# Performance work log

Measured on AMD Instinct MI355X. Metric: run time of the kernel, lower is better.

The kernel has to match this reference:

```python
import jax, jax.numpy as jnp
import numpy as np

N, E, F_IN, HID, NC = 8192, 262144, 128, 64, 10
EPS_BN = 1e-5


def gat_layer(x, edge_src, edge_dst, W, att_src, att_dst, bias, heads):
    # x: [N, Fin]; W: [Fin, heads*C]; att_*: [heads, C]; bias: [C]
    n = x.shape[0]
    h = (x @ W).reshape(n, heads, -1)                     # [N,H,C]
    a_s = (h * att_src).sum(-1)                           # [N,H]
    a_d = (h * att_dst).sum(-1)                           # [N,H]
    e = jax.nn.leaky_relu(a_s[edge_src] + a_d[edge_dst], 0.2)  # [E,H]
    # segment softmax over destination node (self-loops guarantee >=1 edge per dst)
    m = jax.ops.segment_max(e, edge_dst, num_segments=n)
    ex = jnp.exp(e - m[edge_dst])
    s = jax.ops.segment_sum(ex, edge_dst, num_segments=n)
    alpha = ex / (s[edge_dst] + 1e-16)                    # [E,H]
    out = jax.ops.segment_sum(h[edge_src] * alpha[:, :, None], edge_dst, num_segments=n)  # [N,H,C]
    return out.mean(axis=1) + bias                        # concat=False -> mean over heads


def batch_norm(x, gamma, beta):
    mu = x.mean(axis=0)
    var = x.var(axis=0)  # biased, as PyTorch uses for normalization
    return (x - mu) * jax.lax.rsqrt(var + EPS_BN) * gamma + beta


def mha(x, Wq, Wk, Wv, bq, bk, bv, Wo, bo, num_heads=4):
    n, d = x.shape
    hd = d // num_heads
    q = (x @ Wq.T + bq).reshape(n, num_heads, hd)
    k = (x @ Wk.T + bk).reshape(n, num_heads, hd)
    v = (x @ Wv.T + bv).reshape(n, num_heads, hd)
    scores = jnp.einsum('nhd,mhd->hnm', q, k) / jnp.sqrt(jnp.asarray(hd, x.dtype))
    attn = jax.nn.softmax(scores, axis=-1)
    out = jnp.einsum('hnm,mhd->nhd', attn, v).reshape(n, d)
    return out @ Wo.T + bo


def setup_inputs() -> dict:
    key = jax.random.key(0)
    ks = jax.random.split(key, 32)
    d = {}
    d['x'] = jax.random.normal(ks[0], (N, F_IN), dtype=jnp.float32)
    d['edge_index'] = jax.random.randint(ks[1], (2, E), 0, N, dtype=jnp.int32)
    heads_list = [8, 8, 1]
    fins = [F_IN, HID, HID]
    for i, (fin, h) in enumerate(zip(fins, heads_list)):
        sc = 1.0 / np.sqrt(fin)
        d[f'W{i}'] = jax.random.normal(ks[2 + 4 * i], (fin, h * HID), dtype=jnp.float32) * sc
        d[f'as{i}'] = jax.random.normal(ks[3 + 4 * i], (h, HID), dtype=jnp.float32) * 0.1
        d[f'ad{i}'] = jax.random.normal(ks[4 + 4 * i], (h, HID), dtype=jnp.float32) * 0.1
        d[f'b{i}'] = jnp.zeros((HID,), dtype=jnp.float32)
    d['bn_gamma'] = jnp.ones((3, HID), dtype=jnp.float32)
    d['bn_beta'] = jnp.zeros((3, HID), dtype=jnp.float32)
    sc = 1.0 / np.sqrt(HID)
    for j, name in enumerate(['Wq', 'Wk', 'Wv', 'Wo']):
        d[name] = jax.random.normal(ks[16 + j], (HID, HID), dtype=jnp.float32) * sc
    for name in ['bq', 'bk', 'bv', 'bo']:
        d[name] = jnp.zeros((HID,), dtype=jnp.float32)
    d['Wc1'] = jax.random.normal(ks[20], (HID // 2, HID), dtype=jnp.float32) * sc
    d['bc1'] = jnp.zeros((HID // 2,), dtype=jnp.float32)
    d['Wc2'] = jax.random.normal(ks[21], (NC, HID // 2), dtype=jnp.float32) * (1.0 / np.sqrt(HID // 2))
    d['bc2'] = jnp.zeros((NC,), dtype=jnp.float32)
    return d


def reference(x, edge_index, W0, as0, ad0, b0, W1, as1, ad1, b1, W2, as2, ad2, b2,
              bn_gamma, bn_beta, Wq, Wk, Wv, bq, bk, bv, Wo, bo, Wc1, bc1, Wc2, bc2):
    n = x.shape[0]
    # PyG GATConv default add_self_loops=True
    loops = jnp.arange(n, dtype=edge_index.dtype)
    src = jnp.concatenate([edge_index[0], loops])
    dst = jnp.concatenate([edge_index[1], loops])
    heads_list = [8, 8, 1]
    params = [(W0, as0, ad0, b0), (W1, as1, ad1, b1), (W2, as2, ad2, b2)]
    for i in range(3):
        Wl, asl, adl, bl = params[i]
        x = gat_layer(x, src, dst, Wl, asl, adl, bl, heads_list[i])
        x = batch_norm(x, bn_gamma[i], bn_beta[i])
        x = jax.nn.relu(x)  # dropout inactive (eval)
    x = mha(x, Wq, Wk, Wv, bq, bk, bv, Wo, bo)
    x = jax.nn.relu(x @ Wc1.T + bc1)
    return x @ Wc2.T + bc2
```

## Files before the change

### kernel.cpp

```cpp
#include <hip/hip_runtime.h>
#include <hip/hip_bf16.h>

#define NN 8192
#define EE 262144
#define HID 64

typedef _Float16 half4_t __attribute__((ext_vector_type(4)));
typedef _Float16 half8_t __attribute__((ext_vector_type(8)));
typedef float f32x4 __attribute__((ext_vector_type(4)));

extern "C" __device__ float __ocml_native_exp2_f32(float);
#define EXP2N(x) __ocml_native_exp2_f32(x)

#define MFMA16(a, b, c) __builtin_amdgcn_mfma_f32_16x16x16f16(a, b, c, 0, 0, 0)

template<bool TRANS_B, bool OUT_F16, int ACT, bool GAT, bool BN>
__device__ __forceinline__ void mfma_gemm_body(
        const float* __restrict__ A, const float* __restrict__ B,
        const float* __restrict__ bias, void* __restrict__ Cout,
        int M, int Nc, int K, float scale, int brow, int bcol,
        const float* __restrict__ att_s, const float* __restrict__ att_d,
        float* __restrict__ a_s, float* __restrict__ a_d, int H,
        const float* __restrict__ bnsc, const float* __restrict__ bnsh) {
    __shared__ _Float16 Ah[64][36];
    __shared__ _Float16 Bt[64][36];
    int tid  = threadIdx.x;
    int wave = tid >> 6, lane = tid & 63, lo16 = lane & 15, g = lane >> 4;
    f32x4 acc[4];
    #pragma unroll
    for (int i = 0; i < 4; ++i) acc[i] = (f32x4){0.f, 0.f, 0.f, 0.f};

    for (int k0 = 0; k0 < K; k0 += 32) {
        {
            int r  = tid >> 2;
            int ks = (tid & 3) * 8;
            const float* ap = A + (size_t)(brow + r) * K + k0 + ks;
            f32x4 a0 = *(const f32x4*)ap;
            f32x4 a1 = *(const f32x4*)(ap + 4);
            if (BN) {
                #pragma unroll
                for (int i = 0; i < 4; ++i) {
                    int c0 = k0 + ks + i, c1 = c0 + 4;
                    a0[i] = fmaxf(a0[i] * bnsc[c0] + bnsh[c0], 0.f);
                    a1[i] = fmaxf(a1[i] * bnsc[c1] + bnsh[c1], 0.f);
                }
            }
            half4_t h0, h1;
            #pragma unroll
            for (int i = 0; i < 4; ++i) { h0[i] = (_Float16)a0[i]; h1[i] = (_Float16)a1[i]; }
            *(half4_t*)&Ah[r][ks]     = h0;
            *(half4_t*)&Ah[r][ks + 4] = h1;
        }
        if (TRANS_B) {
            int n  = tid >> 2;
            int ks = (tid & 3) * 8;
            const float* bp = B + (size_t)(bcol + n) * K + k0 + ks;
            f32x4 b0 = *(const f32x4*)bp;
            f32x4 b1 = *(const f32x4*)(bp + 4);
            half4_t h0, h1;
            #pragma unroll
            for (int i = 0; i < 4; ++i) { h0[i] = (_Float16)b0[i]; h1[i] = (_Float16)b1[i]; }
            *(half4_t*)&Bt[n][ks]     = h0;
            *(half4_t*)&Bt[n][ks + 4] = h1;
        } else {
            int n  = tid & 63;
            int kb = (tid >> 6) * 8;
            half4_t h0, h1;
            #pragma unroll
            for (int i = 0; i < 4; ++i)
                h0[i] = (_Float16)B[(size_t)(k0 + kb + i) * Nc + bcol + n];
            #pragma unroll
            for (int i = 0; i < 4; ++i)
                h1[i] = (_Float16)B[(size_t)(k0 + kb + 4 + i) * Nc + bcol + n];
            *(half4_t*)&Bt[n][kb]     = h0;
            *(half4_t*)&Bt[n][kb + 4] = h1;
        }
        __syncthreads();
        #pragma unroll
        for (int kh = 0; kh < 2; ++kh) {
            half4_t af = *(const half4_t*)&Ah[wave * 16 + lo16][kh * 16 + g * 4];
            #pragma unroll
            for (int cf = 0; cf < 4; ++cf) {
                half4_t bf = *(const half4_t*)&Bt[cf * 16 + lo16][kh * 16 + g * 4];
                acc[cf] = MFMA16(af, bf, acc[cf]);
            }
        }
        __syncthreads();
    }
    int rbase = brow + wave * 16 + g * 4;
    #pragma unroll
    for (int cf = 0; cf < 4; ++cf) {
        int c = bcol + cf * 16 + lo16;
        float bv = bias ? bias[c] : 0.f;
        #pragma unroll
        for (int reg = 0; reg < 4; ++reg) {
            float v = (acc[cf][reg] + bv) * scale;
            if (ACT == 1) v = fmaxf(v, 0.f);
            if (OUT_F16) ((_Float16*)Cout)[(size_t)(rbase + reg) * Nc + c] = (_Float16)v;
            else         ((float*)Cout)[(size_t)(rbase + reg) * Nc + c] = v;
        }
    }
    if (GAT) {
        float as_c[4], ad_c[4];
        #pragma unroll
        for (int cf = 0; cf < 4; ++cf) {
            int c = bcol + cf * 16 + lo16;
            as_c[cf] = att_s[c];
            ad_c[cf] = att_d[c];
        }
        int head = bcol >> 6;
        #pragma unroll
        for (int reg = 0; reg < 4; ++reg) {
            float ps = 0.f, pd = 0.f;
            #pragma unroll
            for (int cf = 0; cf < 4; ++cf) {
                ps += acc[cf][reg] * as_c[cf];
                pd += acc[cf][reg] * ad_c[cf];
            }
            #pragma unroll
            for (int off = 8; off; off >>= 1) {
                ps += __shfl_xor(ps, off);
                pd += __shfl_xor(pd, off);
            }
            if (lo16 == 0) {
                int row = rbase + reg;
                a_s[row * H + head] = ps;
                a_d[row * H + head] = pd;
            }
        }
    }
}

template<bool TRANS_B, bool OUT_F16, int ACT, bool GAT, bool BN>
__global__ void mfma_gemm(const float* __restrict__ A, const float* __restrict__ B,
                          const float* __restrict__ bias, void* __restrict__ Cout,
                          int M, int Nc, int K, float scale,
                          const float* __restrict__ att_s, const float* __restrict__ att_d,
                          float* __restrict__ a_s, float* __restrict__ a_d, int H,
                          const float* __restrict__ bnsc, const float* __restrict__ bnsh) {
    mfma_gemm_body<TRANS_B, OUT_F16, ACT, GAT, BN>(A, B, bias, Cout, M, Nc, K, scale,
                                                   blockIdx.y * 64, blockIdx.x * 64,
                                                   att_s, att_d, a_s, a_d, H, bnsc, bnsh);
}

__global__ void qkv_gemm(const float* __restrict__ A,
                         const float* __restrict__ Wq, const float* __restrict__ Wk,
                         const float* __restrict__ Wv, const float* __restrict__ bq,
                         const float* __restrict__ bk, const float* __restrict__ bv,
                         _Float16* __restrict__ qh, _Float16* __restrict__ kh,
                         _Float16* __restrict__ vh, int M, float qscale,
                         const float* __restrict__ bnsc, const float* __restrict__ bnsh) {
    int z = blockIdx.z;
    const float* B    = z == 0 ? Wq : (z == 1 ? Wk : Wv);
    const float* bias = z == 0 ? bq : (z == 1 ? bk : bv);
    _Float16* Cout    = z == 0 ? qh : (z == 1 ? kh : vh);
    float scale       = z == 0 ? qscale : 1.f;
    mfma_gemm_body<true, true, 0, false, true>(A, B, bias, Cout, M, 64, 64, scale,
                                               blockIdx.y * 64, 0,
                                               nullptr, nullptr, nullptr, nullptr, 0,
                                               bnsc, bnsh);
}

__global__ void count_deg(const int* __restrict__ ei, int* __restrict__ deg, int E) {
    int e = blockIdx.x * 256 + threadIdx.x;
    if (e < E) atomicAdd(&deg[ei[E + e]], 1);
}

__global__ void scan_deg(const int* __restrict__ deg, int* __restrict__ row_ptr,
                         int* __restrict__ cursor, int N) {
    __shared__ int tmp[1024];
    int tid = threadIdx.x;
    int base = tid * 8;
    int local[8];
    int s = 0;
    #pragma unroll
    for (int j = 0; j < 8; ++j) { local[j] = deg[base + j] + 1; s += local[j]; }
    tmp[tid] = s;
    __syncthreads();
    for (int off = 1; off < 1024; off <<= 1) {
        int add = (tid >= off) ? tmp[tid - off] : 0;
        __syncthreads();
        tmp[tid] += add;
        __syncthreads();
    }
    int run = tmp[tid] - s;
    #pragma unroll
    for (int j = 0; j < 8; ++j) {
        row_ptr[base + j] = run;
        cursor[base + j]  = run;
        run += local[j];
    }
    if (tid == 1023) row_ptr[N] = run;
}

__global__ void fill_csr(const int* __restrict__ ei, int* __restrict__ cursor,
                         int* __restrict__ col, int E, int N) {
    int e = blockIdx.x * 256 + threadIdx.x;
    if (e < E) {
        int dst = ei[E + e];
        int pos = atomicAdd(&cursor[dst], 1);
        col[pos] = ei[e];
    } else if (e < E + N) {
        int n = e - E;
        int pos = atomicAdd(&cursor[n], 1);
        col[pos] = n;
    }
}

__global__ void gat_gather_h8(const _Float16* __restrict__ h, const float* __restrict__ a_s,
                              const float* __restrict__ a_d, const int* __restrict__ row_ptr,
                              const int* __restrict__ col, float* __restrict__ out, int N) {
    __shared__ float wsf[4][64][8];
    __shared__ int   wsc[4][64];
    int t = threadIdx.x, wave = t >> 6, lane = t & 63;
    int n = (blockIdx.x * 256 + t) >> 6;
    int hd = lane >> 3;
    int beg = row_ptr[n], end = row_ptr[n + 1];
    float ad[8];
    #pragma unroll
    for (int i = 0; i < 8; ++i) ad[i] = a_d[n * 8 + i];
    float m[8];
    #pragma unroll
    for (int i = 0; i < 8; ++i) m[i] = -1e30f;
    for (int j = beg + lane; j < end; j += 64) {
        int c = col[j];
        f32x4 s0 = *(const f32x4*)(a_s + (size_t)c * 8);
        f32x4 s1 = *(const f32x4*)(a_s + (size_t)c * 8 + 4);
        #pragma unroll
        for (int i = 0; i < 4; ++i) {
            float sa = s0[i] + ad[i];
            sa = sa > 0.f ? sa : 0.2f * sa;
            m[i] = fmaxf(m[i], sa);
            float sb = s1[i] + ad[4 + i];
            sb = sb > 0.f ? sb : 0.2f * sb;
            m[4 + i] = fmaxf(m[4 + i], sb);
        }
    }
    #pragma unroll
    for (int i = 0; i < 8; ++i)
        #pragma unroll
        for (int off = 32; off; off >>= 1) m[i] = fmaxf(m[i], __shfl_xor(m[i], off));
    const _Float16* hb = h + (size_t)lane * 8;
    float acc[8] = {0.f, 0.f, 0.f, 0.f, 0.f, 0.f, 0.f, 0.f};
    float den[8] = {0.f, 0.f, 0.f, 0.f, 0.f, 0.f, 0.f, 0.f};
    for (int base = beg; base < end; base += 64) {
        int j = base + lane;
        int cj = 0;
        float w[8];
        #pragma unroll
        for (int i = 0; i < 8; ++i) w[i] = 0.f;
        if (j < end) {
            cj = col[j];
            f32x4 s0 = *(const f32x4*)(a_s + (size_t)cj * 8);
            f32x4 s1 = *(const f32x4*)(a_s + (size_t)cj * 8 + 4);
            #pragma unroll
            for (int i = 0; i < 4; ++i) {
                float sa = s0[i] + ad[i];
                sa = sa > 0.f ? sa : 0.2f * sa;
                w[i] = __expf(sa - m[i]);
                den[i] += w[i];
                float sb = s1[i] + ad[4 + i];
                sb = sb > 0.f ? sb : 0.2f * sb;
                w[4 + i] = __expf(sb - m[4 + i]);
                den[4 + i] += w[4 + i];
            }
        }
        wsc[wave][lane] = cj;
        *(f32x4*)&wsf[wave][lane][0] = (f32x4){w[0], w[1], w[2], w[3]};
        *(f32x4*)&wsf[wave][lane][4] = (f32x4){w[4], w[5], w[6], w[7]};
        int cnt = min(64, end - base);
        #pragma unroll 2
        for (int k = 0; k < cnt; ++k) {
            int ck  = wsc[wave][k];
            float wk = wsf[wave][k][hd];
            half8_t hv = *(const half8_t*)(hb + (size_t)ck * 512);
            #pragma unroll
            for (int i = 0; i < 8; ++i) acc[i] += wk * (float)hv[i];
        }
    }
    #pragma unroll
    for (int i = 0; i < 8; ++i)
        #pragma unroll
        for (int off = 32; off; off >>= 1) den[i] += __shfl_xor(den[i], off);
    float inv = 1.f / ((den[hd] + 1e-16f) * 8.f);
    float y[8];
    #pragma unroll
    for (int i = 0; i < 8; ++i) y[i] = acc[i] * inv;
    #pragma unroll
    for (int i = 0; i < 8; ++i) {
        y[i] += __shfl_xor(y[i], 8);
        y[i] += __shfl_xor(y[i], 16);
        y[i] += __shfl_xor(y[i], 32);
    }
    if (lane < 8) {
        *(f32x4*)(out + (size_t)n * 64 + lane * 8)     = (f32x4){y[0], y[1], y[2], y[3]};
        *(f32x4*)(out + (size_t)n * 64 + lane * 8 + 4) = (f32x4){y[4], y[5], y[6], y[7]};
    }
}

__global__ void gat_gather_h1(const _Float16* __restrict__ h, const float* __restrict__ a_s,
                              const float* __restrict__ a_d, const int* __restrict__ row_ptr,
                              const int* __restrict__ col, float* __restrict__ out, int N) {
    __shared__ uint2 wc[4][64];
    int t    = threadIdx.x;
    int wave = t >> 6;
    int lane = t & 63;
    int n    = (blockIdx.x * 256 + t) >> 6;
    int beg = row_ptr[n], end = row_ptr[n + 1];
    float adn = a_d[n];
    float m = -1e30f;
    for (int j = beg + lane; j < end; j += 64) {
        float sc = a_s[col[j]] + adn;
        sc = sc > 0.f ? sc : 0.2f * sc;
        m = fmaxf(m, sc);
    }
    #pragma unroll
    for (int off = 32; off; off >>= 1) m = fmaxf(m, __shfl_xor(m, off));
    const _Float16* hb = h + lane;
    float denom = 0.f;
    float acc0 = 0.f, acc1 = 0.f, acc2 = 0.f, acc3 = 0.f;
    float acc4 = 0.f, acc5 = 0.f, acc6 = 0.f, acc7 = 0.f;
    for (int base = beg; base < end; base += 64) {
        int j = base + lane;
        float w = 0.f; int s = 0;
        if (j < end) {
            s = col[j];
            float sc = a_s[s] + adn;
            sc = sc > 0.f ? sc : 0.2f * sc;
            w = __expf(sc - m);
        }
        denom += w;
        uint2 p; p.x = __float_as_uint(w); p.y = (unsigned)s;
        wc[wave][lane] = p;
        int cnt = min(64, end - base);
        int k = 0;
        for (; k + 8 <= cnt; k += 8) {
            uint2 p0 = wc[wave][k];
            uint2 p1 = wc[wave][k + 1];
            uint2 p2 = wc[wave][k + 2];
            uint2 p3 = wc[wave][k + 3];
            uint2 p4 = wc[wave][k + 4];
            uint2 p5 = wc[wave][k + 5];
            uint2 p6 = wc[wave][k + 6];
            uint2 p7 = wc[wave][k + 7];
            acc0 += __uint_as_float(p0.x) * (float)hb[(size_t)p0.y * 64];
            acc1 += __uint_as_float(p1.x) * (float)hb[(size_t)p1.y * 64];
            acc2 += __uint_as_float(p2.x) * (float)hb[(size_t)p2.y * 64];
            acc3 += __uint_as_float(p3.x) * (float)hb[(size_t)p3.y * 64];
            acc4 += __uint_as_float(p4.x) * (float)hb[(size_t)p4.y * 64];
            acc5 += __uint_as_float(p5.x) * (float)hb[(size_t)p5.y * 64];
            acc6 += __uint_as_float(p6.x) * (float)hb[(size_t)p6.y * 64];
            acc7 += __uint_as_float(p7.x) * (float)hb[(size_t)p7.y * 64];
        }
        for (; k < cnt; ++k) {
            uint2 p0 = wc[wave][k];
            acc0 += __uint_as_float(p0.x) * (float)hb[(size_t)p0.y * 64];
        }
    }
    float acc = ((acc0 + acc1) + (acc2 + acc3)) + ((acc4 + acc5) + (acc6 + acc7));
    #pragma unroll
    for (int off = 32; off; off >>= 1) denom += __shfl_xor(denom, off);
    out[(size_t)n * 64 + lane] = acc / (denom + 1e-16f);
}

__global__ void bn_stats(const float* __restrict__ x, const float* __restrict__ gamma,
                         const float* __restrict__ beta, float* __restrict__ scale,
                         float* __restrict__ shift, int N) {
    int c = blockIdx.x;
    float s = 0.f, ss = 0.f;
    for (int r = threadIdx.x; r < N; r += 256) {
        float v = x[(size_t)r * 64 + c];
        s += v; ss += v * v;
    }
    #pragma unroll
    for (int off = 32; off; off >>= 1) {
        s  += __shfl_xor(s, off);
        ss += __shfl_xor(ss, off);
    }
    __shared__ float red[8];
    int wv = threadIdx.x >> 6, ln = threadIdx.x & 63;
    if (ln == 0) { red[wv] = s; red[4 + wv] = ss; }
    __syncthreads();
    if (threadIdx.x == 0) {
        float S  = red[0] + red[1] + red[2] + red[3];
        float SS = red[4] + red[5] + red[6] + red[7];
        float mu  = S / N;
        float var = SS / N - mu * mu;
        float istd = rsqrtf(var + 1e-5f);
        scale[c] = gamma[c] * istd;
        shift[c] = beta[c] - mu * gamma[c] * istd;
    }
}

__global__ void vkpack(const _Float16* __restrict__ vh, const _Float16* __restrict__ kh,
                       _Float16* __restrict__ vt, _Float16* __restrict__ khp, int N) {
    __shared__ _Float16 tile[64][68];
    int kb = blockIdx.x * 64;
    int t  = threadIdx.x;
    {
        int r = t >> 2, c0 = (t & 3) * 16;
        half8_t x0 = *(const half8_t*)(vh + (size_t)(kb + r) * 64 + c0);
        half8_t x1 = *(const half8_t*)(vh + (size_t)(kb + r) * 64 + c0 + 8);
        #pragma unroll
        for (int i = 0; i < 8; ++i) { tile[r][c0 + i] = x0[i]; tile[r][c0 + 8 + i] = x1[i]; }
    }
    #pragma unroll
    for (int rep = 0; rep < 2; ++rep) {
        int l = t + 256 * rep;
        int n = kb + (l >> 3), c8 = (l & 7) * 8;
        half8_t v = *(const half8_t*)(kh + (size_t)n * 64 + c8);
        *(half8_t*)(khp + ((size_t)(c8 >> 4) * N + n) * 16 + (c8 & 15)) = v;
    }
    __syncthreads();
    {
        int c = t >> 2, ks = (t & 3) * 16;
        half8_t y0, y1;
        #pragma unroll
        for (int i = 0; i < 8; ++i) { y0[i] = tile[ks + i][c]; y1[i] = tile[ks + 8 + i][c]; }
        *(half8_t*)(vt + (size_t)c * N + kb + ks)     = y0;
        *(half8_t*)(vt + (size_t)c * N + kb + ks + 8) = y1;
    }
}

__global__ __launch_bounds__(512) void mha_fa5(const _Float16* __restrict__ qh,
                                               const _Float16* __restrict__ khp,
                                               const _Float16* __restrict__ vt,
                                               float* __restrict__ ao, int N) {
    __shared__ alignas(16) char smem[38912];
    typedef _Float16 (*KtT)[2][64][20];
    typedef _Float16 (*VtT)[2][16][68];
    KtT Kt = (KtT)smem;
    VtT Vt = (VtT)(smem + 20480);
    float* MBp = (float*)(smem + 37888);
    float* OBp = (float*)smem;

    int h    = blockIdx.y;
    int t    = threadIdx.x;
    int lane = t & 63;
    int wave = t >> 6;
    int grp  = wave >> 1;
    int wsub = wave & 1;
    int lo16 = lane & 15;
    int g    = lane >> 4;
    int q    = blockIdx.x * 32 + wsub * 16 + lo16;

    half4_t qf = *(const half4_t*)(qh + (size_t)q * 64 + h * 16 + g * 4);
    const _Float16* kp = khp + (size_t)h * N * 16;
    const _Float16* vp = vt + (size_t)h * 16 * N;

    int gt   = t & 127;
    int skey = gt >> 1, sch = (gt & 1) * 8;
    int sd   = gt >> 3, skv = (gt & 7) * 8;

    {
        int kt = grp * 64;
        half8_t kv = *(const half8_t*)(kp + (size_t)(kt + skey) * 16 + sch);
        half8_t vv = *(const half8_t*)(vp + (size_t)sd * N + kt + skv);
        half4_t a, b, c, d;
        #pragma unroll
        for (int i = 0; i < 4; ++i) { a[i] = kv[i]; b[i] = kv[4 + i]; c[i] = vv[i]; d[i] = vv[4 + i]; }
        *(half4_t*)&Kt[grp][0][skey][sch]     = a;
        *(half4_t*)&Kt[grp][0][skey][sch + 4] = b;
        *(half4_t*)&Vt[grp][0][sd][skv]       = c;
        *(half4_t*)&Vt[grp][0][sd][skv + 4]   = d;
    }

    float m = -1e30f, l = 0.f;
    f32x4 o = {0.f, 0.f, 0.f, 0.f};
    const f32x4 zero = {0.f, 0.f, 0.f, 0.f};
    const int nit = N / 256;

    for (int it = 0; it < nit; ++it) {
        int cur = it & 1;
        __syncthreads();
        if (it + 1 < nit) {
            int kt = ((it + 1) * 4 + grp) * 64;
            half8_t kv = *(const half8_t*)(kp + (size_t)(kt + skey) * 16 + sch);
            half8_t vv = *(const half8_t*)(vp + (size_t)sd * N + kt + skv);
            half4_t a, b, c, d;
            #pragma unroll
            for (int i = 0; i < 4; ++i) { a[i] = kv[i]; b[i] = kv[4 + i]; c[i] = vv[i]; d[i] = vv[4 + i]; }
            *(half4_t*)&Kt[grp][cur ^ 1][skey][sch]     = a;
            *(half4_t*)&Kt[grp][cur ^ 1][skey][sch + 4] = b;
            *(half4_t*)&Vt[grp][cur ^ 1][sd][skv]       = c;
            *(half4_t*)&Vt[grp][cur ^ 1][sd][skv + 4]   = d;
        }
        f32x4 s[4];
        __builtin_amdgcn_s_setprio(1);
        #pragma unroll
        for (int st = 0; st < 4; ++st) {
            half4_t kf = *(const half4_t*)&Kt[grp][cur][st * 16 + lo16][g * 4];
            s[st] = MFMA16(kf, qf, zero);
        }
        __builtin_amdgcn_s_setprio(0);
        float t0 = fmaxf(fmaxf(s[0][0], s[0][1]), s[0][2]);
        float t1 = fmaxf(fmaxf(s[0][3], s[1][0]), s[1][1]);
        float t2 = fmaxf(fmaxf(s[1][2], s[1][3]), s[2][0]);
        float t3 = fmaxf(fmaxf(s[2][1], s[2][2]), s[2][3]);
        float t4 = fmaxf(fmaxf(s[3][0], s[3][1]), fmaxf(s[3][2], s[3][3]));
        float tm = fmaxf(fmaxf(fmaxf(t0, t1), fmaxf(t2, t3)), t4);
        tm = fmaxf(tm, __shfl_xor(tm, 16));
        tm = fmaxf(tm, __shfl_xor(tm, 32));
        if (!__all(tm <= m + 8.f)) {
            float mnew = fmaxf(m, tm);
            float r = EXP2N(m - mnew);
            l *= r;
            #pragma unroll
            for (int i = 0; i < 4; ++i) o[i] *= r;
            m = mnew;
        }
        float lsum = 0.f;
        half4_t pf[4];
        #pragma unroll
        for (int st = 0; st < 4; ++st) {
            float p0 = EXP2N(s[st][0] - m);
            float p1 = EXP2N(s[st][1] - m);
            float p2 = EXP2N(s[st][2] - m);
            float p3 = EXP2N(s[st][3] - m);
            lsum += (p0 + p1) + (p2 + p3);
            auto lo = __builtin_amdgcn_cvt_pkrtz(p0, p1);
            auto hi = __builtin_amdgcn_cvt_pkrtz(p2, p3);
            pf[st][0] = (_Float16)lo[0]; pf[st][1] = (_Float16)lo[1];
            pf[st][2] = (_Float16)hi[0]; pf[st][3] = (_Float16)hi[1];
        }
        l += lsum;
        __builtin_amdgcn_s_setprio(1);
        #pragma unroll
        for (int st = 0; st < 4; ++st) {
            half4_t vf = *(const half4_t*)&Vt[grp][cur][lo16][st * 16 + g * 4];
            o = MFMA16(vf, pf[st], o);
        }
        __builtin_amdgcn_s_setprio(0);
    }
    l += __shfl_xor(l, 16);
    l += __shfl_xor(l, 32);

    __syncthreads();
    if (grp != 0) {
        if (lane < 16) {
            MBp[((wsub * 4 + grp) * 2 + 0) * 16 + lane] = m;
            MBp[((wsub * 4 + grp) * 2 + 1) * 16 + lane] = l;
        }
        #pragma unroll
        for (int i = 0; i < 4; ++i)
            OBp[((wsub * 4 + grp) * 16 + g * 4 + i) * 17 + lo16] = o[i];
    }
    __syncthreads();
    if (grp == 0) {
        float M = m, L = l;
        f32x4 O = o;
        #pragma unroll
        for (int gg = 1; gg < 4; ++gg) {
            float m1 = MBp[((wsub * 4 + gg) * 2 + 0) * 16 + lo16];
            float l1 = MBp[((wsub * 4 + gg) * 2 + 1) * 16 + lo16];
            float Mn = fmaxf(M, m1);
            float e0 = EXP2N(M - Mn), e1 = EXP2N(m1 - Mn);
            L = L * e0 + l1 * e1;
            #pragma unroll
            for (int i = 0; i < 4; ++i)
                O[i] = O[i] * e0 + OBp[((wsub * 4 + gg) * 16 + g * 4 + i) * 17 + lo16] * e1;
            M = Mn;
        }
        float inv = 1.f / L;
        f32x4 res;
        #pragma unroll
        for (int i = 0; i < 4; ++i) res[i] = O[i] * inv;
        *(f32x4*)(ao + (size_t)q * 64 + h * 16 + g * 4) = res;
    }
}

__global__ void mlp_head(const float* __restrict__ ao,
                         const float* __restrict__ Wo, const float* __restrict__ bo,
                         const float* __restrict__ Wc1, const float* __restrict__ bc1,
                         const float* __restrict__ Wc2, const float* __restrict__ bc2,
                         float* __restrict__ outp, int N) {
    __shared__ _Float16 At[64][68];
    __shared__ _Float16 Bt[64][68];
    int t = threadIdx.x, wave = t >> 6, lane = t & 63, lo16 = lane & 15, g = lane >> 4;
    int brow = blockIdx.x * 64;
    const f32x4 zero = {0.f, 0.f, 0.f, 0.f};
    {
        int r = t >> 2, c0 = (t & 3) * 16;
        const float* ap = ao + (size_t)(brow + r) * 64 + c0;
        const float* wp = Wo + (size_t)r * 64 + c0;
        #pragma unroll
        for (int j = 0; j < 16; j += 4) {
            f32x4 va = *(const f32x4*)(ap + j);
            f32x4 vw = *(const f32x4*)(wp + j);
            half4_t ha, hw;
            #pragma unroll
            for (int i = 0; i < 4; ++i) { ha[i] = (_Float16)va[i]; hw[i] = (_Float16)vw[i]; }
            *(half4_t*)&At[r][c0 + j] = ha;
            *(half4_t*)&Bt[r][c0 + j] = hw;
        }
    }
    __syncthreads();
    f32x4 acc1[4];
    #pragma unroll
    for (int i = 0; i < 4; ++i) acc1[i] = zero;
    #pragma unroll
    for (int kc = 0; kc < 4; ++kc) {
        half4_t af = *(const half4_t*)&At[wave * 16 + lo16][kc * 16 + g * 4];
        #pragma unroll
        for (int cf = 0; cf < 4; ++cf) {
            half4_t bf = *(const half4_t*)&Bt[cf * 16 + lo16][kc * 16 + g * 4];
            acc1[cf] = MFMA16(af, bf, acc1[cf]);
        }
    }
    #pragma unroll
    for (int cf = 0; cf < 4; ++cf) {
        int c = cf * 16 + lo16;
        float bv = bo[c];
        #pragma unroll
        for (int reg = 0; reg < 4; ++reg)
            At[wave * 16 + g * 4 + reg][c] = (_Float16)(acc1[cf][reg] + bv);
    }
    __syncthreads();
    {
        int r = t >> 2, c0 = (t & 3) * 16;
        if (r < 32) {
            const float* wp = Wc1 + (size_t)r * 64 + c0;
            #pragma unroll
            for (int j = 0; j < 16; j += 4) {
                f32x4 vw = *(const f32x4*)(wp + j);
                half4_t hw;
                #pragma unroll
                for (int i = 0; i < 4; ++i) hw[i] = (_Float16)vw[i];
                *(half4_t*)&Bt[r][c0 + j] = hw;
            }
        }
    }
    __syncthreads();
    f32x4 acc2[2];
    acc2[0] = zero; acc2[1] = zero;
    #pragma unroll
    for (int kc = 0; kc < 4; ++kc) {
        half4_t af = *(const half4_t*)&At[wave * 16 + lo16][kc * 16 + g * 4];
        #pragma unroll
        for (int cf = 0; cf < 2; ++cf) {
            half4_t bf = *(const half4_t*)&Bt[cf * 16 + lo16][kc * 16 + g * 4];
            acc2[cf] = MFMA16(af, bf, acc2[cf]);
        }
    }
    #pragma unroll
    for (int cf = 0; cf < 2; ++cf) {
        int c = cf * 16 + lo16;
        float bv = bc1[c];
        #pragma unroll
        for (int reg = 0; reg < 4; ++reg)
            At[wave * 16 + g * 4 + reg][c] = (_Float16)fmaxf(acc2[cf][reg] + bv, 0.f);
    }
    __syncthreads();
    {
        if (t < 32) {
            int r = t >> 1, c0 = (t & 1) * 16;
            half4_t hw;
            #pragma unroll
            for (int j = 0; j < 16; j += 4) {
                if (r < 10) {
                    f32x4 vw = *(const f32x4*)(Wc2 + (size_t)r * 32 + c0 + j);
                    #pragma unroll
                    for (int i = 0; i < 4; ++i) hw[i] = (_Float16)vw[i];
                } else {
                    #pragma unroll
                    for (int i = 0; i < 4; ++i) hw[i] = (_Float16)0.f;
                }
                *(half4_t*)&Bt[r][c0 + j] = hw;
            }
        }
    }
    __syncthreads();
    f32x4 acc3 = zero;
    #pragma unroll
    for (int kc = 0; kc < 2; ++kc) {
        half4_t af = *(const half4_t*)&At[wave * 16 + lo16][kc * 16 + g * 4];
        half4_t bf = *(const half4_t*)&Bt[lo16][kc * 16 + g * 4];
        acc3 = MFMA16(af, bf, acc3);
    }
    if (lo16 < 10) {
        float bv = bc2[lo16];
        #pragma unroll
        for (int reg = 0; reg < 4; ++reg) {
            int row = brow + wave * 16 + g * 4 + reg;
            outp[(size_t)row * 10 + lo16] = acc3[reg] + bv;
        }
    }
}

extern "C" void kernel_launch(void* const* d_in, const int* in_sizes, int n_in,
                              void* d_out, int out_size, void* d_ws, size_t ws_size,
                              hipStream_t stream) {
    const int N = NN, E = EE;
    const float* x    = (const float*)d_in[0];
    const int*   ei   = (const int*)d_in[1];
    const float* W[3]   = {(const float*)d_in[2], (const float*)d_in[6], (const float*)d_in[10]};
    const float* as_[3] = {(const float*)d_in[3], (const float*)d_in[7], (const float*)d_in[11]};
    const float* ad_[3] = {(const float*)d_in[4], (const float*)d_in[8], (const float*)d_in[12]};
    const float* bn_g = (const float*)d_in[14];
    const float* bn_b = (const float*)d_in[15];
    const float* Wq = (const float*)d_in[16];
    const float* Wk = (const float*)d_in[17];
    const float* Wv = (const float*)d_in[18];
    const float* Wo = (const float*)d_in[19];
    const float* bq = (const float*)d_in[20];
    const float* bk = (const float*)d_in[21];
    const float* bv = (const float*)d_in[22];
    const float* bo = (const float*)d_in[23];
    const float* Wc1 = (const float*)d_in[24];
    const float* bc1 = (const float*)d_in[25];
    const float* Wc2 = (const float*)d_in[26];
    const float* bc2 = (const float*)d_in[27];

    char* ws = (char*)d_ws;
    _Float16* h16 = (_Float16*)(ws + 0);
    _Float16* qh = (_Float16*)(ws + 9437184);
    _Float16* kh = (_Float16*)(ws + 10485760);
    _Float16* vh = (_Float16*)(ws + 11534336);
    _Float16* vt = (_Float16*)(ws + 12582912);
    _Float16* khp = (_Float16*)(ws + 13631488);
    float* a_s  = (float*)(ws + 16777216);
    float* a_d  = (float*)(ws + 17039360);
    int* row_ptr = (int*)(ws + 17301504);
    int* cursor  = (int*)(ws + 17334528);
    int* deg     = (int*)(ws + 17367296);
    int* col     = (int*)(ws + 17400064);
    float* g0   = (float*)(ws + 18481408);
    float* g1   = (float*)(ws + 20578560);
    float* ao   = (float*)(ws + 28967168);
    float* bnscale = (float*)(ws + 32112896);
    float* bnshift = bnscale + 64;

    hipMemsetAsync(deg, 0, (size_t)N * 4, stream);
    count_deg<<<(E + 255) / 256, 256, 0, stream>>>(ei, deg, E);
    scan_deg<<<1, 1024, 0, stream>>>(deg, row_ptr, cursor, N);
    fill_csr<<<(E + N + 255) / 256, 256, 0, stream>>>(ei, cursor, col, E, N);

    mfma_gemm<false, true, 0, true, false><<<dim3(8, N / 64), 256, 0, stream>>>(
        x, W[0], nullptr, h16, N, 512, 128, 1.f, as_[0], ad_[0], a_s, a_d, 8, nullptr, nullptr);
    gat_gather_h8<<<N / 4, 256, 0, stream>>>(h16, a_s, a_d, row_ptr, col, g0, N);
    bn_stats<<<64, 256, 0, stream>>>(g0, bn_g, bn_b, bnscale, bnshift, N);
    mfma_gemm<false, true, 0, true, true><<<dim3(8, N / 64), 256, 0, stream>>>(
        g0, W[1], nullptr, h16, N, 512, 64, 1.f, as_[1], ad_[1], a_s, a_d, 8, bnscale, bnshift);
    gat_gather_h8<<<N / 4, 256, 0, stream>>>(h16, a_s, a_d, row_ptr, col, g1, N);
    bn_stats<<<64, 256, 0, stream>>>(g1, bn_g + 64, bn_b + 64, bnscale, bnshift, N);
    mfma_gemm<false, true, 0, true, true><<<dim3(1, N / 64), 256, 0, stream>>>(
        g1, W[2], nullptr, h16, N, 64, 64, 1.f, as_[2], ad_[2], a_s, a_d, 1, bnscale, bnshift);
    gat_gather_h1<<<N / 4, 256, 0, stream>>>(h16, a_s, a_d, row_ptr, col, g0, N);
    bn_stats<<<64, 256, 0, stream>>>(g0, bn_g + 128, bn_b + 128, bnscale, bnshift, N);

    qkv_gemm<<<dim3(1, N / 64, 3), 256, 0, stream>>>(
        g0, Wq, Wk, Wv, bq, bk, bv, qh, kh, vh, N, 0.36067376f, bnscale, bnshift);
    vkpack<<<N / 64, 256, 0, stream>>>(vh, kh, vt, khp, N);
    mha_fa5<<<dim3(N / 32, 4), 512, 0, stream>>>(qh, khp, vt, ao, N);

    mlp_head<<<N / 64, 256, 0, stream>>>(ao, Wo, bo, Wc1, bc1, Wc2, bc2, (float*)d_out, N);
}
```

Baseline: 268.2 us.

## Split GAT gather per node across four waves with online softmax merge

New measurement: 315.9 us. 1.18x slower.

```diff
diff --git a/kernel.cpp b/kernel.cpp
--- a/kernel.cpp
+++ b/kernel.cpp
@@ -207,72 +207,85 @@
     }
 }
 
-__global__ void gat_gather_h8(const _Float16* __restrict__ h, const float* __restrict__ a_s,
-                              const float* __restrict__ a_d, const int* __restrict__ row_ptr,
-                              const int* __restrict__ col, float* __restrict__ out, int N) {
+__global__ __launch_bounds__(256) void gat_gather_h8(
+        const _Float16* __restrict__ h, const float* __restrict__ a_s,
+        const float* __restrict__ a_d, const int* __restrict__ row_ptr,
+        const int* __restrict__ col, float* __restrict__ out, int N) {
     __shared__ float wsf[4][64][8];
     __shared__ int   wsc[4][64];
-    int t = threadIdx.x, wave = t >> 6, lane = t & 63;
-    int n = (blockIdx.x * 256 + t) >> 6;
+    __shared__ float MD[4][2][8];
+    int t = threadIdx.x, w = t >> 6, lane = t & 63;
+    int n = blockIdx.x;
     int hd = lane >> 3;
     int beg = row_ptr[n], end = row_ptr[n + 1];
+    int deg = end - beg;
+    int cw = (deg - w + 3) >> 2;
     float ad[8];
     #pragma unroll
     for (int i = 0; i < 8; ++i) ad[i] = a_d[n * 8 + i];
-    float m[8];
-    #pragma unroll
-    for (int i = 0; i < 8; ++i) m[i] = -1e30f;
-    for (int j = beg + lane; j < end; j += 64) {
-        int c = col[j];
-        f32x4 s0 = *(const f32x4*)(a_s + (size_t)c * 8);
-        f32x4 s1 = *(const f32x4*)(a_s + (size_t)c * 8 + 4);
-        #pragma unroll
-        for (int i = 0; i < 4; ++i) {
-            float sa = s0[i] + ad[i];
-            sa = sa > 0.f ? sa : 0.2f * sa;
-            m[i] = fmaxf(m[i], sa);
-            float sb = s1[i] + ad[4 + i];
-            sb = sb > 0.f ? sb : 0.2f * sb;
-            m[4 + i] = fmaxf(m[4 + i], sb);
-        }
-    }
-    #pragma unroll
-    for (int i = 0; i < 8; ++i)
-        #pragma unroll
-        for (int off = 32; off; off >>= 1) m[i] = fmaxf(m[i], __shfl_xor(m[i], off));
+    float m[8], den[8], acc[8];
+    #pragma unroll
+    for (int i = 0; i < 8; ++i) { m[i] = -1e30f; den[i] = 0.f; acc[i] = 0.f; }
     const _Float16* hb = h + (size_t)lane * 8;
-    float acc[8] = {0.f, 0.f, 0.f, 0.f, 0.f, 0.f, 0.f, 0.f};
-    float den[8] = {0.f, 0.f, 0.f, 0.f, 0.f, 0.f, 0.f, 0.f};
-    for (int base = beg; base < end; base += 64) {
-        int j = base + lane;
+
+    for (int base = 0; base < cw; base += 64) {
+        int k = base + lane;
+        bool valid = k < cw;
         int cj = 0;
-        float w[8];
-        #pragma unroll
-        for (int i = 0; i < 8; ++i) w[i] = 0.f;
-        if (j < end) {
-            cj = col[j];
+        float sc[8];
+        #pragma unroll
+        for (int i = 0; i < 8; ++i) sc[i] = -1e30f;
+        if (valid) {
+            cj = col[beg + w + 4 * k];
             f32x4 s0 = *(const f32x4*)(a_s + (size_t)cj * 8);
             f32x4 s1 = *(const f32x4*)(a_s + (size_t)cj * 8 + 4);
             #pragma unroll
             for (int i = 0; i < 4; ++i) {
                 float sa = s0[i] + ad[i];
-                sa = sa > 0.f ? sa : 0.2f * sa;
-                w[i] = __expf(sa - m[i]);
-                den[i] += w[i];
+                sc[i] = sa > 0.f ? sa : 0.2f * sa;
                 float sb = s1[i] + ad[4 + i];
-                sb = sb > 0.f ? sb : 0.2f * sb;
-                w[4 + i] = __expf(sb - m[4 + i]);
-                den[4 + i] += w[4 + i];
-            }
-        }
-        wsc[wave][lane] = cj;
-        *(f32x4*)&wsf[wave][lane][0] = (f32x4){w[0], w[1], w[2], w[3]};
-        *(f32x4*)&wsf[wave][lane][4] = (f32x4){w[4], w[5], w[6], w[7]};
-        int cnt = min(64, end - base);
-        #pragma unroll 2
-        for (int k = 0; k < cnt; ++k) {
-            int ck  = wsc[wave][k];
-            float wk = wsf[wave][k][hd];
+                sc[4 + i] = sb > 0.f ? sb : 0.2f * sb;
+            }
+        }
+        float cm[8];
+        #pragma unroll
+        for (int i = 0; i < 8; ++i) {
+            cm[i] = sc[i];
+            #pragma unroll
+            for (int off = 32; off; off >>= 1) cm[i] = fmaxf(cm[i], __shfl_xor(cm[i], off));
+        }
+        if (base > 0) {
+            float r[8];
+            #pragma unroll
+            for (int i = 0; i < 8; ++i) {
+                float mn = fmaxf(m[i], cm[i]);
+                r[i] = __expf(m[i] - mn);
+                den[i] *= r[i];
+                m[i] = mn;
+            }
+            float rh = r[0];
+            #pragma unroll
+            for (int i = 1; i < 8; ++i) rh = (hd == i) ? r[i] : rh;
+            #pragma unroll
+            for (int i = 0; i < 8; ++i) acc[i] *= rh;
+        } else {
+            #pragma unroll
+            for (int i = 0; i < 8; ++i) m[i] = cm[i];
+        }
+        float wv[8];
+        #pragma unroll
+        for (int i = 0; i < 8; ++i) {
+            wv[i] = valid ? __expf(sc[i] - m[i]) : 0.f;
+            den[i] += wv[i];
+        }
+        wsc[w][lane] = cj;
+        *(f32x4*)&wsf[w][lane][0] = (f32x4){wv[0], wv[1], wv[2], wv[3]};
+        *(f32x4*)&wsf[w][lane][4] = (f32x4){wv[4], wv[5], wv[6], wv[7]};
+        int cnt = min(64, cw - base);
+        #pragma unroll 4
+        for (int k2 = 0; k2 < cnt; ++k2) {
+            int ck   = wsc[w][k2];
+            float wk = wsf[w][k2][hd];
             half8_t hv = *(const half8_t*)(hb + (size_t)ck * 512);
             #pragma unroll
             for (int i = 0; i < 8; ++i) acc[i] += wk * (float)hv[i];
@@ -282,85 +295,104 @@
     for (int i = 0; i < 8; ++i)
         #pragma unroll
         for (int off = 32; off; off >>= 1) den[i] += __shfl_xor(den[i], off);
-    float inv = 1.f / ((den[hd] + 1e-16f) * 8.f);
-    float y[8];
-    #pragma unroll
-    for (int i = 0; i < 8; ++i) y[i] = acc[i] * inv;
-    #pragma unroll
-    for (int i = 0; i < 8; ++i) {
-        y[i] += __shfl_xor(y[i], 8);
-        y[i] += __shfl_xor(y[i], 16);
-        y[i] += __shfl_xor(y[i], 32);
-    }
-    if (lane < 8) {
-        *(f32x4*)(out + (size_t)n * 64 + lane * 8)     = (f32x4){y[0], y[1], y[2], y[3]};
-        *(f32x4*)(out + (size_t)n * 64 + lane * 8 + 4) = (f32x4){y[4], y[5], y[6], y[7]};
-    }
-}
-
-__global__ void gat_gather_h1(const _Float16* __restrict__ h, const float* __restrict__ a_s,
-                              const float* __restrict__ a_d, const int* __restrict__ row_ptr,
-                              const int* __restrict__ col, float* __restrict__ out, int N) {
+    *(f32x4*)&wsf[w][lane][0] = (f32x4){acc[0], acc[1], acc[2], acc[3]};
+    *(f32x4*)&wsf[w][lane][4] = (f32x4){acc[4], acc[5], acc[6], acc[7]};
+    if (lane == 0) {
+        #pragma unroll
+        for (int i = 0; i < 8; ++i) { MD[w][0][i] = m[i]; MD[w][1][i] = den[i]; }
+    }
+    __syncthreads();
+    if (w == 0) {
+        float M = fmaxf(fmaxf(MD[0][0][hd], MD[1][0][hd]), fmaxf(MD[2][0][hd], MD[3][0][hd]));
+        float f0 = __expf(MD[0][0][hd] - M);
+        float f1 = __expf(MD[1][0][hd] - M);
+        float f2 = __expf(MD[2][0][hd] - M);
+        float f3 = __expf(MD[3][0][hd] - M);
+        float D = MD[0][1][hd] * f0 + MD[1][1][hd] * f1 + MD[2][1][hd] * f2 + MD[3][1][hd] * f3;
+        float y[8];
+        #pragma unroll
+        for (int i = 0; i < 8; ++i)
+            y[i] = wsf[0][lane][i] * f0 + wsf[1][lane][i] * f1 +
+                   wsf[2][lane][i] * f2 + wsf[3][lane][i] * f3;
+        float inv = 1.f / ((D + 1e-16f) * 8.f);
+        #pragma unroll
+        for (int i = 0; i < 8; ++i) y[i] *= inv;
+        #pragma unroll
+        for (int i = 0; i < 8; ++i) {
+            y[i] += __shfl_xor(y[i], 8);
+            y[i] += __shfl_xor(y[i], 16);
+            y[i] += __shfl_xor(y[i], 32);
+        }
+        if (lane < 8) {
+            *(f32x4*)(out + (size_t)n * 64 + lane * 8)     = (f32x4){y[0], y[1], y[2], y[3]};
+            *(f32x4*)(out + (size_t)n * 64 + lane * 8 + 4) = (f32x4){y[4], y[5], y[6], y[7]};
+        }
+    }
+}
+
+__global__ __launch_bounds__(256) void gat_gather_h1(
+        const _Float16* __restrict__ h, const float* __restrict__ a_s,
+        const float* __restrict__ a_d, const int* __restrict__ row_ptr,
+        const int* __restrict__ col, float* __restrict__ out, int N) {
     __shared__ uint2 wc[4][64];
-    int t    = threadIdx.x;
-    int wave = t >> 6;
-    int lane = t & 63;
-    int n    = (blockIdx.x * 256 + t) >> 6;
+    __shared__ float wacc[4][64];
+    __shared__ float MD1[4][2];
+    int t = threadIdx.x, w = t >> 6, lane = t & 63;
+    int n = blockIdx.x;
     int beg = row_ptr[n], end = row_ptr[n + 1];
+    int deg = end - beg;
+    int cw = (deg - w + 3) >> 2;
     float adn = a_d[n];
-    float m = -1e30f;
-    for (int j = beg + lane; j < end; j += 64) {
-        float sc = a_s[col[j]] + adn;
-        sc = sc > 0.f ? sc : 0.2f * sc;
-        m = fmaxf(m, sc);
-    }
-    #pragma unroll
-    for (int off = 32; off; off >>= 1) m = fmaxf(m, __shfl_xor(m, off));
+    float m = -1e30f, den = 0.f, acc = 0.f;
     const _Float16* hb = h + lane;
-    float denom = 0.f;
-    float acc0 = 0.f, acc1 = 0.f, acc2 = 0.f, acc3 = 0.f;
-    float acc4 = 0.f, acc5 = 0.f, acc6 = 0.f, acc7 = 0.f;
-    for (int base = beg; base < end; base += 64) {
-        int j = base + lane;
-        float w = 0.f; int s = 0;
-        if (j < end) {
-            s = col[j];
-            float sc = a_s[s] + adn;
-            sc = sc > 0.f ? sc : 0.2f * sc;
-            w = __expf(sc - m);
-        }
-        denom += w;
-        uint2 p; p.x = __float_as_uint(w); p.y = (unsigned)s;
-        wc[wave][lane] = p;
-        int cnt = min(64, end - base);
-        int k = 0;
-        for (; k + 8 <= cnt; k += 8) {
-            uint2 p0 = wc[wave][k];
-            uint2 p1 = wc[wave][k + 1];
-            uint2 p2 = wc[wave][k + 2];
-            uint2 p3 = wc[wave][k + 3];
-            uint2 p4 = wc[wave][k + 4];
-            uint2 p5 = wc[wave][k + 5];
-            uint2 p6 = wc[wave][k + 6];
-            uint2 p7 = wc[wave][k + 7];
-            acc0 += __uint_as_float(p0.x) * (float)hb[(size_t)p0.y * 64];
-            acc1 += __uint_as_float(p1.x) * (float)hb[(size_t)p1.y * 64];
-            acc2 += __uint_as_float(p2.x) * (float)hb[(size_t)p2.y * 64];
-            acc3 += __uint_as_float(p3.x) * (float)hb[(size_t)p3.y * 64];
-            acc4 += __uint_as_float(p4.x) * (float)hb[(size_t)p4.y * 64];
-            acc5 += __uint_as_float(p5.x) * (float)hb[(size_t)p5.y * 64];
-            acc6 += __uint_as_float(p6.x) * (float)hb[(size_t)p6.y * 64];
-            acc7 += __uint_as_float(p7.x) * (float)hb[(size_t)p7.y * 64];
-        }
-        for (; k < cnt; ++k) {
-            uint2 p0 = wc[wave][k];
-            acc0 += __uint_as_float(p0.x) * (float)hb[(size_t)p0.y * 64];
-        }
-    }
-    float acc = ((acc0 + acc1) + (acc2 + acc3)) + ((acc4 + acc5) + (acc6 + acc7));
-    #pragma unroll
-    for (int off = 32; off; off >>= 1) denom += __shfl_xor(denom, off);
-    out[(size_t)n * 64 + lane] = acc / (denom + 1e-16f);
+
+    for (int base = 0; base < cw; base += 64) {
+        int k = base + lane;
+        bool valid = k < cw;
+        int cj = 0;
+        float sc = -1e30f;
+        if (valid) {
+            cj = col[beg + w + 4 * k];
+            float sa = a_s[cj] + adn;
+            sc = sa > 0.f ? sa : 0.2f * sa;
+        }
+        float cm = sc;
+        #pragma unroll
+        for (int off = 32; off; off >>= 1) cm = fmaxf(cm, __shfl_xor(cm, off));
+        if (base > 0) {
+            float mn = fmaxf(m, cm);
+            float r = __expf(m - mn);
+            den *= r; acc *= r; m = mn;
+        } else {
+            m = cm;
+        }
+        float wv = valid ? __expf(sc - m) : 0.f;
+        den += wv;
+        uint2 p; p.x = __float_as_uint(wv); p.y = (unsigned)cj;
+        wc[w][lane] = p;
+        int cnt = min(64, cw - base);
+        #pragma unroll 4
+        for (int k2 = 0; k2 < cnt; ++k2) {
+            uint2 q = wc[w][k2];
+            acc += __uint_as_float(q.x) * (float)hb[(size_t)q.y * 64];
+        }
+    }
+    #pragma unroll
+    for (int off = 32; off; off >>= 1) den += __shfl_xor(den, off);
+    wacc[w][lane] = acc;
+    if (lane == 0) { MD1[w][0] = m; MD1[w][1] = den; }
+    __syncthreads();
+    if (w == 0) {
+        float M = fmaxf(fmaxf(MD1[0][0], MD1[1][0]), fmaxf(MD1[2][0], MD1[3][0]));
+        float D = 0.f, y = 0.f;
+        #pragma unroll
+        for (int w2 = 0; w2 < 4; ++w2) {
+            float f = __expf(MD1[w2][0] - M);
+            D += MD1[w2][1] * f;
+            y += wacc[w2][lane] * f;
+        }
+        out[(size_t)n * 64 + lane] = y / (D + 1e-16f);
+    }
 }
 
 __global__ void bn_stats(const float* __restrict__ x, const float* __restrict__ gamma,
@@ -737,15 +769,15 @@
 
     mfma_gemm<false, true, 0, true, false><<<dim3(8, N / 64), 256, 0, stream>>>(
         x, W[0], nullptr, h16, N, 512, 128, 1.f, as_[0], ad_[0], a_s, a_d, 8, nullptr, nullptr);
-    gat_gather_h8<<<N / 4, 256, 0, stream>>>(h16, a_s, a_d, row_ptr, col, g0, N);
+    gat_gather_h8<<<N, 256, 0, stream>>>(h16, a_s, a_d, row_ptr, col, g0, N);
     bn_stats<<<64, 256, 0, stream>>>(g0, bn_g, bn_b, bnscale, bnshift, N);
     mfma_gemm<false, true, 0, true, true><<<dim3(8, N / 64), 256, 0, stream>>>(
         g0, W[1], nullptr, h16, N, 512, 64, 1.f, as_[1], ad_[1], a_s, a_d, 8, bnscale, bnshift);
-    gat_gather_h8<<<N / 4, 256, 0, stream>>>(h16, a_s, a_d, row_ptr, col, g1, N);
+    gat_gather_h8<<<N, 256, 0, stream>>>(h16, a_s, a_d, row_ptr, col, g1, N);
     bn_stats<<<64, 256, 0, stream>>>(g1, bn_g + 64, bn_b + 64, bnscale, bnshift, N);
     mfma_gemm<false, true, 0, true, true><<<dim3(1, N / 64), 256, 0, stream>>>(
         g1, W[2], nullptr, h16, N, 64, 64, 1.f, as_[2], ad_[2], a_s, a_d, 1, bnscale, bnshift);
-    gat_gather_h1<<<N / 4, 256, 0, stream>>>(h16, a_s, a_d, row_ptr, col, g0, N);
+    gat_gather_h1<<<N, 256, 0, stream>>>(h16, a_s, a_d, row_ptr, col, g0, N);
     bn_stats<<<64, 256, 0, stream>>>(g0, bn_g + 128, bn_b + 128, bnscale, bnshift, N);
 
     qkv_gemm<<<dim3(1, N / 64, 3), 256, 0, stream>>>(
```
